# Performance work log

Hardware: AMD Instinct MI355X
Metric: run time of the kernel (lower is better)

The kernel has to match this reference:

```python
import jax, jax.numpy as jnp
import numpy as np

D_MODEL = 1024
N_HEADS = 16
D_K = D_MODEL // N_HEADS
THETA = 10000.0
MAX_SEQ_LEN = 2048


def _rope_tables(seq_len):
    pos = jnp.arange(seq_len, dtype=jnp.float32)
    inv_freq = 1.0 / (THETA ** (jnp.arange(0, D_K, 2, dtype=jnp.float32) / D_K))
    ang = pos[:, None] * inv_freq[None, :]  # [T, D_K/2]
    return jnp.cos(ang), jnp.sin(ang)


def _apply_rope(x, cos, sin):
    # x: [..., T, D_K]; cos/sin: [T, D_K/2]
    x_even = x[..., ::2]
    x_odd = x[..., 1::2]
    r_even = x_even * cos - x_odd * sin
    r_odd = x_even * sin + x_odd * cos
    out = jnp.stack([r_even, r_odd], axis=-1)  # [..., T, D_K/2, 2]
    return out.reshape(x.shape)


def setup_inputs() -> dict:
    key = jax.random.key(0)
    ks = jax.random.split(key, 5)
    std = np.sqrt(2.0 / (D_MODEL + D_MODEL))
    x = jax.random.normal(ks[0], (2, 2048, D_MODEL), dtype=jnp.float32)
    w_q = jax.random.normal(ks[1], (D_MODEL, D_MODEL), dtype=jnp.float32) * std
    w_k = jax.random.normal(ks[2], (D_MODEL, D_MODEL), dtype=jnp.float32) * std
    w_v = jax.random.normal(ks[3], (D_MODEL, D_MODEL), dtype=jnp.float32) * std
    w_o = jax.random.normal(ks[4], (D_MODEL, D_MODEL), dtype=jnp.float32) * std
    return {"x": x, "w_q": w_q, "w_k": w_k, "w_v": w_v, "w_o": w_o}


def reference(x, w_q, w_k, w_v, w_o):
    B, T, _ = x.shape
    # projections: weight stored as [d_out, d_in], y = x @ W^T
    q = jnp.einsum('btd,od->bto', x, w_q)
    k = jnp.einsum('btd,od->bto', x, w_k)
    v = jnp.einsum('btd,od->bto', x, w_v)
    # split heads: [B, T, H*Dk] -> [B, H, T, Dk]
    q = q.reshape(B, T, N_HEADS, D_K).transpose(0, 2, 1, 3)
    k = k.reshape(B, T, N_HEADS, D_K).transpose(0, 2, 1, 3)
    v = v.reshape(B, T, N_HEADS, D_K).transpose(0, 2, 1, 3)
    cos, sin = _rope_tables(T)
    q = _apply_rope(q, cos, sin)
    k = _apply_rope(k, cos, sin)
    scores = jnp.einsum('bhqd,bhkd->bhqk', q, k) / np.sqrt(D_K).astype(np.float32)
    causal = jnp.tril(jnp.ones((T, T), dtype=bool))
    scores = jnp.where(causal, scores, -jnp.inf)
    attn = jax.nn.softmax(scores, axis=-1)
    out = jnp.einsum('bhqk,bhkd->bhqd', attn, v)
    out = out.transpose(0, 2, 1, 3).reshape(B, T, D_MODEL)
    return jnp.einsum('btd,od->bto', out, w_o)
```

## Files before the change

### kernel.cpp

```cpp
#include <hip/hip_runtime.h>
#include <hip/hip_bf16.h>

typedef __bf16 bf16_t;
typedef __bf16 bf16x8 __attribute__((ext_vector_type(8)));
typedef float f32x4 __attribute__((ext_vector_type(4)));
typedef short short4v __attribute__((ext_vector_type(4)));

#define D_MODEL 1024
#define T_SEQ 2048
#define NH 16
#define DKD 64
#define X_ELEMS (4194304u)
#define W_ELEMS (1048576u)

__device__ __forceinline__ void async16(const bf16_t* g, bf16_t* l) {
    __builtin_amdgcn_global_load_lds((const __attribute__((address_space(1))) void*)g,
                                     (__attribute__((address_space(3))) void*)l, 16, 0, 0);
}

__global__ __launch_bounds__(256) void convert_kernel(
    const float* __restrict__ x, const float* __restrict__ wq,
    const float* __restrict__ wk, const float* __restrict__ wv,
    const float* __restrict__ wo,
    bf16_t* __restrict__ xb, bf16_t* __restrict__ wqb, bf16_t* __restrict__ wkb,
    bf16_t* __restrict__ wvb, bf16_t* __restrict__ wob)
{
    size_t idx = ((size_t)blockIdx.x * 256 + threadIdx.x) * 4;
    const float* src; bf16_t* dst; size_t off;
    if (idx < X_ELEMS) { src = x; dst = xb; off = idx; }
    else {
        size_t r = idx - X_ELEMS;
        unsigned w = (unsigned)(r >> 20);
        off = r & (W_ELEMS - 1);
        src = (w == 0) ? wq : (w == 1) ? wk : (w == 2) ? wv : wo;
        dst = (w == 0) ? wqb : (w == 1) ? wkb : (w == 2) ? wvb : wob;
    }
    float4 v = *(const float4*)(src + off);
    union { bf16_t b[4]; short4v s; } u;
    u.b[0] = (bf16_t)v.x; u.b[1] = (bf16_t)v.y;
    u.b[2] = (bf16_t)v.z; u.b[3] = (bf16_t)v.w;
    *(short4v*)(dst + off) = u.s;
}

__global__ __launch_bounds__(256) void rope_kernel(float* __restrict__ cost, float* __restrict__ sint)
{
    int idx = blockIdx.x * 256 + threadIdx.x;
    int t = idx >> 5, i = idx & 31;
    float inv = expf(-0.28782313662425572f * (float)i);
    float ang = (float)t * inv;
    float s, c;
    sincosf(ang, &s, &c);
    cost[idx] = c; sint[idx] = s;
}

__global__ __launch_bounds__(256) void gemm_fused(
    const bf16_t* __restrict__ A,
    const bf16_t* __restrict__ W0, const bf16_t* __restrict__ W1, const bf16_t* __restrict__ W2,
    bf16_t* __restrict__ qout, bf16_t* __restrict__ kout, bf16_t* __restrict__ vout,
    const float* __restrict__ cost, const float* __restrict__ sint,
    float* __restrict__ fout, int modeBase)
{
    const int K = 1024;
    __shared__ bf16_t As[128 * 32];
    __shared__ bf16_t Bs[128 * 32];
    const int tid = threadIdx.x;
    const int wave = tid >> 6, lane = tid & 63;
    const int quad = lane >> 4, l16 = lane & 15;
    const int m0 = blockIdx.x * 128;
    const int n0 = blockIdx.y * 128;
    const int wm = (wave >> 1) * 64, wn = (wave & 1) * 64;
    const int mode = modeBase + blockIdx.z;
    const bf16_t* W = (mode == 1) ? W1 : (mode == 2) ? W2 : W0;

    const f32x4 fzero = {0.f, 0.f, 0.f, 0.f};
    f32x4 acc[4][4];
    #pragma unroll
    for (int i = 0; i < 4; ++i)
        #pragma unroll
        for (int j = 0; j < 4; ++j) acc[i][j] = fzero;

    for (int k0 = 0; k0 < K; k0 += 32) {
        __syncthreads();
        #pragma unroll
        for (int c = 0; c < 2; ++c) {
            int G = c * 256 + tid;
            int row = G >> 2, go = G & 3;
            async16(A + (size_t)(m0 + row) * K + (k0 + go * 8), As + (size_t)(c * 256 + wave * 64) * 8);
            async16(W + (size_t)(n0 + row) * K + (k0 + go * 8), Bs + (size_t)(c * 256 + wave * 64) * 8);
        }
        __syncthreads();
        bf16x8 af[4], bfv[4];
        #pragma unroll
        for (int mi = 0; mi < 4; ++mi)
            af[mi] = *(const bf16x8*)(As + (wm + mi * 16 + l16) * 32 + quad * 8);
        #pragma unroll
        for (int ni = 0; ni < 4; ++ni)
            bfv[ni] = *(const bf16x8*)(Bs + (wn + ni * 16 + l16) * 32 + quad * 8);
        #pragma unroll
        for (int mi = 0; mi < 4; ++mi)
            #pragma unroll
            for (int ni = 0; ni < 4; ++ni)
                acc[mi][ni] = __builtin_amdgcn_mfma_f32_16x16x32_bf16(af[mi], bfv[ni], acc[mi][ni], 0, 0, 0);
    }

    #pragma unroll
    for (int mi = 0; mi < 4; ++mi) {
        #pragma unroll
        for (int ni = 0; ni < 4; ++ni) {
            #pragma unroll
            for (int reg = 0; reg < 4; ++reg) {
                int row = m0 + wm + mi * 16 + quad * 4 + reg;
                int col = n0 + wn + ni * 16 + l16;
                float v = acc[mi][ni][reg];
                if (mode == 3) {
                    fout[(size_t)row * D_MODEL + col] = v;
                } else {
                    int t = row & (T_SEQ - 1), b = row >> 11;
                    int h = col >> 6, dk = col & 63;
                    if (mode == 2) {
                        vout[(((size_t)b * NH + h) * DKD + dk) * T_SEQ + t] = (bf16_t)v;
                    } else {
                        float vp = __shfl_xor(v, 1);
                        int fi = dk >> 1;
                        float c = cost[t * 32 + fi], s = sint[t * 32 + fi];
                        float r = (dk & 1) ? (vp * s + v * c) : (v * c - vp * s);
                        bf16_t* dst = (mode == 0) ? qout : kout;
                        dst[(((size_t)b * NH + h) * T_SEQ + t) * DKD + dk] = (bf16_t)r;
                    }
                }
            }
        }
    }
}

__global__ __launch_bounds__(256, 2) void attn_kernel(
    const bf16_t* __restrict__ Q, const bf16_t* __restrict__ Kb,
    const bf16_t* __restrict__ Vt, bf16_t* __restrict__ O)
{
    __shared__ bf16_t Ks[64 * 64];
    __shared__ bf16_t Vs[64 * 64];
    __shared__ bf16_t Pw[4][16 * 72];
    const int tid = threadIdx.x;
    const int wave = tid >> 6, lane = tid & 63;
    const int quad = lane >> 4, l16 = lane & 15;
    const int qb = (int)(gridDim.x - 1) - (int)blockIdx.x;
    const int bh = blockIdx.y;
    const int qw = qb * 128 + wave * 32;

    const bf16_t* kbase = Kb + (size_t)bh * T_SEQ * DKD;
    const bf16_t* vbase = Vt + (size_t)bh * DKD * T_SEQ;

    bf16x8 qf[2][2];
    #pragma unroll
    for (int j = 0; j < 2; ++j) {
        const bf16_t* qp = Q + ((size_t)bh * T_SEQ + qw + j * 16 + l16) * DKD;
        qf[j][0] = *(const bf16x8*)(qp + quad * 8);
        qf[j][1] = *(const bf16x8*)(qp + 32 + quad * 8);
    }
    const f32x4 fzero = {0.f, 0.f, 0.f, 0.f};
    f32x4 oacc[2][4];
    #pragma unroll
    for (int j = 0; j < 2; ++j)
        #pragma unroll
        for (int i = 0; i < 4; ++i) oacc[j][i] = fzero;
    float mrun[2] = {-__builtin_inff(), -__builtin_inff()};
    float lrun[2] = {0.f, 0.f};

    bf16_t* pw = &Pw[wave][0];
    const int nkt = 2 * qb + 2;
    for (int kt = 0; kt < nkt; ++kt) {
        const int k0 = kt * 64;
        __syncthreads();
        #pragma unroll
        for (int c = 0; c < 2; ++c) {
            int G = c * 256 + tid;
            int row = G >> 3, p = G & 7;
            int go = p ^ (row & 7);
            async16(kbase + (size_t)(k0 + row) * DKD + go * 8, Ks + (size_t)(c * 256 + wave * 64) * 8);
            async16(vbase + (size_t)row * T_SEQ + k0 + go * 8, Vs + (size_t)(c * 256 + wave * 64) * 8);
        }
        __syncthreads();
        if (k0 > qw + 31) continue;

        bf16x8 kf[4][2], vf[4][2];
        #pragma unroll
        for (int fi = 0; fi < 4; ++fi) {
            int r = fi * 16 + l16;
            #pragma unroll
            for (int ks = 0; ks < 2; ++ks) {
                int p = (ks * 4 + quad) ^ (r & 7);
                kf[fi][ks] = *(const bf16x8*)(Ks + r * 64 + p * 8);
                vf[fi][ks] = *(const bf16x8*)(Vs + r * 64 + p * 8);
            }
        }

        #pragma unroll
        for (int j = 0; j < 2; ++j) {
            const int qcol = qw + j * 16 + l16;
            if (k0 > qw + j * 16 + 15) continue;

            f32x4 s[4];
            #pragma unroll
            for (int fi = 0; fi < 4; ++fi) {
                f32x4 z = fzero;
                z = __builtin_amdgcn_mfma_f32_16x16x32_bf16(kf[fi][0], qf[j][0], z, 0, 0, 0);
                z = __builtin_amdgcn_mfma_f32_16x16x32_bf16(kf[fi][1], qf[j][1], z, 0, 0, 0);
                s[fi] = z;
            }
            float tm = -__builtin_inff();
            #pragma unroll
            for (int fi = 0; fi < 4; ++fi) {
                #pragma unroll
                for (int reg = 0; reg < 4; ++reg) {
                    float v = s[fi][reg] * 0.125f;
                    int key = k0 + fi * 16 + quad * 4 + reg;
                    v = (key > qcol) ? -__builtin_inff() : v;
                    s[fi][reg] = v;
                    tm = fmaxf(tm, v);
                }
            }
            tm = fmaxf(tm, __shfl_xor(tm, 16));
            tm = fmaxf(tm, __shfl_xor(tm, 32));
            float mnew = fmaxf(mrun[j], tm);
            float alpha = __expf(mrun[j] - mnew);
            mrun[j] = mnew;
            float sm = 0.f;
            #pragma unroll
            for (int fi = 0; fi < 4; ++fi) {
                #pragma unroll
                for (int reg = 0; reg < 4; ++reg) {
                    float p = __expf(s[fi][reg] - mnew);
                    s[fi][reg] = p;
                    sm += p;
                }
            }
            sm += __shfl_xor(sm, 16);
            sm += __shfl_xor(sm, 32);
            lrun[j] = lrun[j] * alpha + sm;
            #pragma unroll
            for (int di = 0; di < 4; ++di)
                #pragma unroll
                for (int reg = 0; reg < 4; ++reg) oacc[j][di][reg] *= alpha;

            #pragma unroll
            for (int fi = 0; fi < 4; ++fi) {
                union { bf16_t h[4]; unsigned long long u64; } pk;
                pk.h[0] = (bf16_t)s[fi][0]; pk.h[1] = (bf16_t)s[fi][1];
                pk.h[2] = (bf16_t)s[fi][2]; pk.h[3] = (bf16_t)s[fi][3];
                *(unsigned long long*)(pw + l16 * 72 + fi * 16 + quad * 4) = pk.u64;
            }
            bf16x8 pf[2];
            pf[0] = *(const bf16x8*)(pw + l16 * 72 + quad * 8);
            pf[1] = *(const bf16x8*)(pw + l16 * 72 + 32 + quad * 8);

            #pragma unroll
            for (int di = 0; di < 4; ++di) {
                oacc[j][di] = __builtin_amdgcn_mfma_f32_16x16x32_bf16(vf[di][0], pf[0], oacc[j][di], 0, 0, 0);
                oacc[j][di] = __builtin_amdgcn_mfma_f32_16x16x32_bf16(vf[di][1], pf[1], oacc[j][di], 0, 0, 0);
            }
        }
    }

    const int b = bh >> 4, h = bh & 15;
    #pragma unroll
    for (int j = 0; j < 2; ++j) {
        float rl = 1.0f / lrun[j];
        int q = qw + j * 16 + l16;
        #pragma unroll
        for (int di = 0; di < 4; ++di) {
            union { bf16_t hh[4]; unsigned long long u64; } ok;
            #pragma unroll
            for (int reg = 0; reg < 4; ++reg) ok.hh[reg] = (bf16_t)(oacc[j][di][reg] * rl);
            int d = di * 16 + quad * 4;
            *(unsigned long long*)(O + ((size_t)b * T_SEQ + q) * D_MODEL + h * DKD + d) = ok.u64;
        }
    }
}

extern "C" void kernel_launch(void* const* d_in, const int* in_sizes, int n_in,
                              void* d_out, int out_size, void* d_ws, size_t ws_size,
                              hipStream_t stream)
{
    const float* x  = (const float*)d_in[0];
    const float* wq = (const float*)d_in[1];
    const float* wk = (const float*)d_in[2];
    const float* wv = (const float*)d_in[3];
    const float* wo = (const float*)d_in[4];
    float* out = (float*)d_out;

    char* ws = (char*)d_ws;
    size_t off = 0;
    auto alloc = [&](size_t bytes) -> void* {
        void* p = ws + off; off += (bytes + 255) & ~(size_t)255; return p;
    };
    bf16_t* xb   = (bf16_t*)alloc((size_t)X_ELEMS * 2);
    bf16_t* wqb  = (bf16_t*)alloc((size_t)W_ELEMS * 2);
    bf16_t* wkb  = (bf16_t*)alloc((size_t)W_ELEMS * 2);
    bf16_t* wvb  = (bf16_t*)alloc((size_t)W_ELEMS * 2);
    bf16_t* wob  = (bf16_t*)alloc((size_t)W_ELEMS * 2);
    bf16_t* qb   = (bf16_t*)alloc((size_t)X_ELEMS * 2);
    bf16_t* kb   = (bf16_t*)alloc((size_t)X_ELEMS * 2);
    bf16_t* vtb  = (bf16_t*)alloc((size_t)X_ELEMS * 2);
    bf16_t* ob   = (bf16_t*)alloc((size_t)X_ELEMS * 2);
    float*  cost = (float*)alloc((size_t)T_SEQ * 32 * 4);
    float*  sint = (float*)alloc((size_t)T_SEQ * 32 * 4);

    convert_kernel<<<8192, 256, 0, stream>>>(x, wq, wk, wv, wo, xb, wqb, wkb, wvb, wob);
    rope_kernel<<<256, 256, 0, stream>>>(cost, sint);
    gemm_fused<<<dim3(32, 8, 3), 256, 0, stream>>>(xb, wqb, wkb, wvb, qb, kb, vtb, cost, sint, nullptr, 0);
    attn_kernel<<<dim3(16, 32), 256, 0, stream>>>(qb, kb, vtb, ob);
    gemm_fused<<<dim3(32, 8, 1), 256, 0, stream>>>(ob, wob, nullptr, nullptr, nullptr, nullptr, nullptr,
                                                   cost, sint, out, 3);
}
```

Baseline: 228.2 us.

## Double-buffer K/V tiles in attention and transpose V-projection MFMA for coalesced stores

The attention kernel now uses two LDS buffers for K and V. It issues the async global-to-LDS load of the next key tile before computing on the current one, which overlaps memory latency with MFMA work and cuts the barriers per iteration from two to one. The V projection swaps its MFMA operands so each accumulator row is a feature and each column a token. That makes the transposed V writes contiguous along the sequence dimension instead of strided. The cost is double the K/V shared memory in attention, which may affect occupancy, and a few extra branch-selected pointers in the GEMM.

```diff
diff --git a/kernel.cpp b/kernel.cpp
--- a/kernel.cpp
+++ b/kernel.cpp
@@ -72,6 +72,11 @@
     const int mode = modeBase + blockIdx.z;
     const bf16_t* W = (mode == 1) ? W1 : (mode == 2) ? W2 : W0;
 
+    const bf16_t* Afrag = (mode == 2) ? Bs : As;
+    const bf16_t* Bfrag = (mode == 2) ? As : Bs;
+    const int aoff = (mode == 2) ? wn : wm;
+    const int boff = (mode == 2) ? wm : wn;
+
     const f32x4 fzero = {0.f, 0.f, 0.f, 0.f};
     f32x4 acc[4][4];
     #pragma unroll
@@ -92,10 +97,10 @@
         bf16x8 af[4], bfv[4];
         #pragma unroll
         for (int mi = 0; mi < 4; ++mi)
-            af[mi] = *(const bf16x8*)(As + (wm + mi * 16 + l16) * 32 + quad * 8);
+            af[mi] = *(const bf16x8*)(Afrag + (aoff + mi * 16 + l16) * 32 + quad * 8);
         #pragma unroll
         for (int ni = 0; ni < 4; ++ni)
-            bfv[ni] = *(const bf16x8*)(Bs + (wn + ni * 16 + l16) * 32 + quad * 8);
+            bfv[ni] = *(const bf16x8*)(Bfrag + (boff + ni * 16 + l16) * 32 + quad * 8);
         #pragma unroll
         for (int mi = 0; mi < 4; ++mi)
             #pragma unroll
@@ -109,17 +114,21 @@
         for (int ni = 0; ni < 4; ++ni) {
             #pragma unroll
             for (int reg = 0; reg < 4; ++reg) {
-                int row = m0 + wm + mi * 16 + quad * 4 + reg;
-                int col = n0 + wn + ni * 16 + l16;
                 float v = acc[mi][ni][reg];
-                if (mode == 3) {
-                    fout[(size_t)row * D_MODEL + col] = v;
+                if (mode == 2) {
+                    int f   = n0 + wn + mi * 16 + quad * 4 + reg;
+                    int tok = m0 + wm + ni * 16 + l16;
+                    int t = tok & (T_SEQ - 1), b = tok >> 11;
+                    int h = f >> 6, dk = f & 63;
+                    vout[(((size_t)b * NH + h) * DKD + dk) * T_SEQ + t] = (bf16_t)v;
                 } else {
-                    int t = row & (T_SEQ - 1), b = row >> 11;
-                    int h = col >> 6, dk = col & 63;
-                    if (mode == 2) {
-                        vout[(((size_t)b * NH + h) * DKD + dk) * T_SEQ + t] = (bf16_t)v;
+                    int row = m0 + wm + mi * 16 + quad * 4 + reg;
+                    int col = n0 + wn + ni * 16 + l16;
+                    if (mode == 3) {
+                        fout[(size_t)row * D_MODEL + col] = v;
                     } else {
+                        int t = row & (T_SEQ - 1), b = row >> 11;
+                        int h = col >> 6, dk = col & 63;
                         float vp = __shfl_xor(v, 1);
                         int fi = dk >> 1;
                         float c = cost[t * 32 + fi], s = sint[t * 32 + fi];
@@ -137,8 +146,8 @@
     const bf16_t* __restrict__ Q, const bf16_t* __restrict__ Kb,
     const bf16_t* __restrict__ Vt, bf16_t* __restrict__ O)
 {
-    __shared__ bf16_t Ks[64 * 64];
-    __shared__ bf16_t Vs[64 * 64];
+    __shared__ bf16_t Ks[2][64 * 64];
+    __shared__ bf16_t Vs[2][64 * 64];
     __shared__ bf16_t Pw[4][16 * 72];
     const int tid = threadIdx.x;
     const int wave = tid >> 6, lane = tid & 63;
@@ -168,19 +177,29 @@
 
     bf16_t* pw = &Pw[wave][0];
     const int nkt = 2 * qb + 2;
-    for (int kt = 0; kt < nkt; ++kt) {
+
+    auto stage = [&](int kt, int buf) {
         const int k0 = kt * 64;
-        __syncthreads();
         #pragma unroll
         for (int c = 0; c < 2; ++c) {
             int G = c * 256 + tid;
             int row = G >> 3, p = G & 7;
             int go = p ^ (row & 7);
-            async16(kbase + (size_t)(k0 + row) * DKD + go * 8, Ks + (size_t)(c * 256 + wave * 64) * 8);
-            async16(vbase + (size_t)row * T_SEQ + k0 + go * 8, Vs + (size_t)(c * 256 + wave * 64) * 8);
-        }
+            async16(kbase + (size_t)(k0 + row) * DKD + go * 8,
+                    &Ks[buf][0] + (size_t)(c * 256 + wave * 64) * 8);
+            async16(vbase + (size_t)row * T_SEQ + k0 + go * 8,
+                    &Vs[buf][0] + (size_t)(c * 256 + wave * 64) * 8);
+        }
+    };
+
+    stage(0, 0);
+    for (int kt = 0; kt < nkt; ++kt) {
         __syncthreads();
+        if (kt + 1 < nkt) stage(kt + 1, (kt + 1) & 1);
+        const int k0 = kt * 64;
         if (k0 > qw + 31) continue;
+        const bf16_t* Kc = &Ks[kt & 1][0];
+        const bf16_t* Vc = &Vs[kt & 1][0];
 
         bf16x8 kf[4][2], vf[4][2];
         #pragma unroll
@@ -189,8 +208,8 @@
             #pragma unroll
             for (int ks = 0; ks < 2; ++ks) {
                 int p = (ks * 4 + quad) ^ (r & 7);
-                kf[fi][ks] = *(const bf16x8*)(Ks + r * 64 + p * 8);
-                vf[fi][ks] = *(const bf16x8*)(Vs + r * 64 + p * 8);
+                kf[fi][ks] = *(const bf16x8*)(Kc + r * 64 + p * 8);
+                vf[fi][ks] = *(const bf16x8*)(Vc + r * 64 + p * 8);
             }
         }
 
```

After: 222.3 us. 1.03x faster.
